# Optimization experiments

Hardware: AMD Instinct MI355X
Metric: run time of the kernel (lower is better)

Reference implementation:

```python
import jax, jax.numpy as jnp
import numpy as np

B, K, N, F, H = 20000, 10, 100000, 256, 128


def setup_inputs() -> dict:
    key = jax.random.key(0)
    ks = jax.random.split(key, 8)
    neighbors = jax.random.randint(ks[0], (B, K), 0, N)
    embed_table = jax.random.normal(ks[1], (N, F), dtype=jnp.float32)
    w = lambda k, shp: jax.random.normal(k, shp, dtype=jnp.float32) * 0.05
    return {
        "neighbors": neighbors,
        "embed_table": embed_table,
        "W1a": w(ks[2], (F, H)), "W1b": w(ks[3], (H, H)),
        "W2a": w(ks[4], (F, H)), "W2b": w(ks[5], (H, H)),
        "W3a": w(ks[6], (F, H)), "W3b": w(ks[7], (H, H)),
    }


def reference(neighbors, embed_table, W1a, W1b, W2a, W2b, W3a, W3b):
    # Gather each batch node's K sampled neighbor embeddings: [B, K, F]
    x = embed_table[neighbors]
    # Three MLP projections: Linear(F,H,no bias) -> tanh -> Linear(H,H,no bias)
    q = jnp.tanh(x @ W1a) @ W1b              # [B, K, H]  (att1)
    k = jnp.tanh(x @ W2a) @ W2b              # [B, K, H]  (att2)
    v = jnp.tanh(x @ W3a) @ W3b              # [B, K, H]  (att3)
    # Per-node attention over the K neighbors, softmax along last dim
    att = jax.nn.softmax(jnp.einsum('bid,bjd->bij', q, k), axis=-1)  # [B, K, K]
    # torch: sum over rows of (att @ v) -> contract both i and j
    out = jnp.einsum('bij,bjd->bd', att, v)  # [B, H]
    return out
```

## Files before the change

### kernel.cpp

```cpp
#include <hip/hip_runtime.h>
#include <hip/hip_bf16.h>

constexpr int B_ = 20000;
constexpr int K_ = 10;
constexpr int N_ = 100000;
constexpr int F_ = 256;
constexpr int H_ = 128;
constexpr int RW = 3 * H_;

typedef __attribute__((ext_vector_type(8))) short bf16x8;
typedef __attribute__((ext_vector_type(4))) float f32x4;
typedef __attribute__((ext_vector_type(4))) unsigned short ushort4v;

__device__ __forceinline__ unsigned short f2bf(float x) {
  unsigned int u = __builtin_bit_cast(unsigned int, x);
  unsigned int r = u + 0x7fffu + ((u >> 16) & 1u);
  return (unsigned short)(r >> 16);
}

__device__ __forceinline__ float bf2f(unsigned int u16) {
  return __builtin_bit_cast(float, u16 << 16);
}

__device__ __forceinline__ float fast_tanh(float x) {
  float e = __expf(2.0f * x);
  return 1.0f - 2.0f * __builtin_amdgcn_rcpf(e + 1.0f);
}

__global__ __launch_bounds__(256) void prep_kernel(
    const float* __restrict__ W1a, const float* __restrict__ W1b,
    const float* __restrict__ W2a, const float* __restrict__ W2b,
    const float* __restrict__ W3a, const float* __restrict__ W3b,
    unsigned short* __restrict__ wat2, unsigned short* __restrict__ wbt2) {
  const float* Wa[3] = {W1a, W2a, W3a};
  const float* Wb[3] = {W1b, W2b, W3b};
  int g = blockIdx.x * 256 + threadIdx.x;
  if (g < 3 * 64 * 512) {
    int chunk = g >> 9;
    int e = g & 511;
    int lane = e >> 3, j = e & 7;
    int c = chunk & 7;
    int ks = (chunk >> 3) & 7;
    int p = chunk >> 6;
    int k = 32 * ks + 8 * (lane >> 4) + j;
    int h = 16 * c + (lane & 15);
    wat2[g] = f2bf(Wa[p][k * H_ + h]);
  } else {
    int g2 = g - 3 * 64 * 512;
    int chunk = g2 >> 9;
    int e = g2 & 511;
    int lane = e >> 3, j = e & 7;
    int ks2 = chunk & 3;
    int c2 = (chunk >> 2) & 7;
    int p = chunk >> 5;
    int k = 32 * ks2 + 8 * (lane >> 4) + j;
    int h2 = 16 * c2 + (lane & 15);
    wbt2[g2] = f2bf(Wb[p][k * H_ + h2]);
  }
}

constexpr int MT = 64;
constexpr int XS = F_ + 8;
constexpr int TS = H_ + 8;

__global__ __launch_bounds__(512, 6) void proj_kernel(
    const float* __restrict__ E,
    const unsigned short* __restrict__ wat2,
    const unsigned short* __restrict__ wbt2,
    unsigned short* __restrict__ qkvI) {
  __shared__ unsigned short xs[MT * XS];
  __shared__ unsigned short ts[MT * TS];

  const int tid = threadIdx.x;
  const int lane = tid & 63;
  const int w = tid >> 6;
  const int l15 = lane & 15;
  const int q = lane >> 4;
  const int row0 = blockIdx.x * MT;

  {
    const float4* Eg = (const float4*)E;
#pragma unroll
    for (int it = 0; it < 8; ++it) {
      int i = tid + 512 * it;
      int r = i >> 6;
      int c4 = i & 63;
      int row = row0 + r;
      if (row >= N_) row = N_ - 1;
      float4 v = Eg[(size_t)row * (F_ / 4) + c4];
      ushort4v o;
      o.x = f2bf(v.x); o.y = f2bf(v.y); o.z = f2bf(v.z); o.w = f2bf(v.w);
      *(ushort4v*)&xs[r * XS + c4 * 4] = o;
    }
  }
  __syncthreads();

  for (int p = 0; p < 3; ++p) {
    const unsigned short* __restrict__ wa = wat2 + p * (64 * 512);
    const unsigned short* __restrict__ wb = wbt2 + p * (32 * 512);

    f32x4 acc[4];
#pragma unroll
    for (int nt = 0; nt < 4; ++nt) acc[nt] = (f32x4)0.0f;

#pragma unroll
    for (int ks = 0; ks < 8; ++ks) {
      bf16x8 af = *(const bf16x8*)&wa[(ks * 8 + w) * 512 + lane * 8];
#pragma unroll
      for (int nt = 0; nt < 4; ++nt) {
        bf16x8 bx = *(const bf16x8*)&xs[(16 * nt + l15) * XS + 32 * ks + 8 * q];
        acc[nt] = __builtin_amdgcn_mfma_f32_16x16x32_bf16(af, bx, acc[nt], 0, 0, 0);
      }
    }

    __syncthreads();
#pragma unroll
    for (int nt = 0; nt < 4; ++nt) {
      ushort4v o;
      o.x = f2bf(fast_tanh(acc[nt][0]));
      o.y = f2bf(fast_tanh(acc[nt][1]));
      o.z = f2bf(fast_tanh(acc[nt][2]));
      o.w = f2bf(fast_tanh(acc[nt][3]));
      *(ushort4v*)&ts[(16 * nt + l15) * TS + 16 * w + 4 * q] = o;
    }
    __syncthreads();

    f32x4 ac2[4];
#pragma unroll
    for (int nt = 0; nt < 4; ++nt) ac2[nt] = (f32x4)0.0f;

#pragma unroll
    for (int ks2 = 0; ks2 < 4; ++ks2) {
      bf16x8 ab = *(const bf16x8*)&wb[(w * 4 + ks2) * 512 + lane * 8];
#pragma unroll
      for (int nt = 0; nt < 4; ++nt) {
        bf16x8 bt = *(const bf16x8*)&ts[(16 * nt + l15) * TS + 32 * ks2 + 8 * q];
        ac2[nt] = __builtin_amdgcn_mfma_f32_16x16x32_bf16(ab, bt, ac2[nt], 0, 0, 0);
      }
    }

#pragma unroll
    for (int nt = 0; nt < 4; ++nt) {
      int n = row0 + 16 * nt + l15;
      if (n < N_) {
        ushort4v o;
        o.x = f2bf(ac2[nt][0]);
        o.y = f2bf(ac2[nt][1]);
        o.z = f2bf(ac2[nt][2]);
        o.w = f2bf(ac2[nt][3]);
        *(ushort4v*)&qkvI[(size_t)n * RW + p * H_ + 16 * w + 4 * q] = o;
      }
    }
  }
}

__global__ __launch_bounds__(256) void agg_kernel(
    const int* __restrict__ nbr,
    const unsigned short* __restrict__ qkvI,
    float* __restrict__ out) {
  const int lane = threadIdx.x & 63;
  const int wv = threadIdx.x >> 6;
  const int b = blockIdx.x * 4 + wv;
  const int l15 = lane & 15;
  const int kg = lane >> 4;

  const int ni = nbr[b * K_ + (l15 < K_ ? l15 : 0)];
  const size_t nbase = (size_t)ni * RW;

  f32x4 sc = (f32x4)0.0f;
#pragma unroll
  for (int k = 0; k < 4; ++k) {
    const int off = k * 32 + kg * 8;
    bf16x8 qf = *(const bf16x8*)&qkvI[nbase + off];
    bf16x8 kf = *(const bf16x8*)&qkvI[nbase + H_ + off];
    sc = __builtin_amdgcn_mfma_f32_16x16x32_bf16(qf, kf, sc, 0, 0, 0);
  }

  if (l15 >= K_) {
#pragma unroll
    for (int r = 0; r < 4; ++r) sc[r] = -3.0e38f;
  }

  float mx[4], e[4], sm[4];
#pragma unroll
  for (int r = 0; r < 4; ++r) mx[r] = sc[r];
#pragma unroll
  for (int st = 1; st < 16; st <<= 1)
#pragma unroll
    for (int r = 0; r < 4; ++r) mx[r] = fmaxf(mx[r], __shfl_xor(mx[r], st, 16));
#pragma unroll
  for (int r = 0; r < 4; ++r) { e[r] = __expf(sc[r] - mx[r]); sm[r] = e[r]; }
#pragma unroll
  for (int st = 1; st < 16; st <<= 1)
#pragma unroll
    for (int r = 0; r < 4; ++r) sm[r] += __shfl_xor(sm[r], st, 16);

  float cs = 0.0f;
#pragma unroll
  for (int r = 0; r < 4; ++r) {
    float a = e[r] * __builtin_amdgcn_rcpf(sm[r]);
    if (kg * 4 + r >= K_) a = 0.0f;
    cs += a;
  }
  cs += __shfl_xor(cs, 16, 64);
  cs += __shfl_xor(cs, 32, 64);

  float o0 = 0.0f, o1 = 0.0f;
#pragma unroll
  for (int j = 0; j < K_; ++j) {
    const float cj = __shfl(cs, j, 64);
    const int nj = __shfl(ni, j, 64);
    const unsigned int v2 =
        *(const unsigned int*)&qkvI[(size_t)nj * RW + 2 * H_ + 2 * lane];
    o0 = fmaf(cj, bf2f(v2 & 0xffffu), o0);
    o1 = fmaf(cj, bf2f(v2 >> 16), o1);
  }
  *(float2*)&out[(size_t)b * H_ + 2 * lane] = make_float2(o0, o1);
}

extern "C" void kernel_launch(void* const* d_in, const int* in_sizes, int n_in,
                              void* d_out, int out_size, void* d_ws, size_t ws_size,
                              hipStream_t stream) {
  const int* nbr = (const int*)d_in[0];
  const float* E = (const float*)d_in[1];
  const float* W1a = (const float*)d_in[2];
  const float* W1b = (const float*)d_in[3];
  const float* W2a = (const float*)d_in[4];
  const float* W2b = (const float*)d_in[5];
  const float* W3a = (const float*)d_in[6];
  const float* W3b = (const float*)d_in[7];
  float* out = (float*)d_out;

  unsigned short* qkvI = (unsigned short*)d_ws;
  unsigned short* wat2 = qkvI + (size_t)N_ * RW;
  unsigned short* wbt2 = wat2 + (size_t)3 * 64 * 512;

  prep_kernel<<<(3 * 64 * 512 + 3 * 32 * 512) / 256, 256, 0, stream>>>(
      W1a, W1b, W2a, W2b, W3a, W3b, wat2, wbt2);
  proj_kernel<<<(N_ + MT - 1) / MT, 512, 0, stream>>>(E, wat2, wbt2, qkvI);
  agg_kernel<<<B_ / 4, 256, 0, stream>>>(nbr, qkvI, out);
}
```

Measured before the change: 236.0 us.

## Software-pipeline projection loop and use packed bf16 conversion instruction

The first-layer GEMM for projection p+1 now runs right after the second-layer GEMM for projection p, so the MFMA work of the next stage overlaps the global stores of the current one and one barrier per iteration is dropped. The manual round-to-nearest bf16 conversion is replaced with the hardware v_cvt_pk_bf16_f32 instruction, which packs two values at once. The launch-bounds occupancy hint of 6 is removed, letting the compiler use more registers at the cost of possibly fewer resident waves.

```diff
diff --git a/kernel.cpp b/kernel.cpp
--- a/kernel.cpp
+++ b/kernel.cpp
@@ -10,7 +10,6 @@
 
 typedef __attribute__((ext_vector_type(8))) short bf16x8;
 typedef __attribute__((ext_vector_type(4))) float f32x4;
-typedef __attribute__((ext_vector_type(4))) unsigned short ushort4v;
 
 __device__ __forceinline__ unsigned short f2bf(float x) {
   unsigned int u = __builtin_bit_cast(unsigned int, x);
@@ -20,6 +19,12 @@
 
 __device__ __forceinline__ float bf2f(unsigned int u16) {
   return __builtin_bit_cast(float, u16 << 16);
+}
+
+__device__ __forceinline__ unsigned int cvt_pk_bf16(float lo, float hi) {
+  unsigned int r;
+  asm("v_cvt_pk_bf16_f32 %0, %1, %2" : "=v"(r) : "v"(lo), "v"(hi));
+  return r;
 }
 
 __device__ __forceinline__ float fast_tanh(float x) {
@@ -63,7 +68,7 @@
 constexpr int XS = F_ + 8;
 constexpr int TS = H_ + 8;
 
-__global__ __launch_bounds__(512, 6) void proj_kernel(
+__global__ __launch_bounds__(512) void proj_kernel(
     const float* __restrict__ E,
     const unsigned short* __restrict__ wat2,
     const unsigned short* __restrict__ wbt2,
@@ -88,21 +93,19 @@
       int row = row0 + r;
       if (row >= N_) row = N_ - 1;
       float4 v = Eg[(size_t)row * (F_ / 4) + c4];
-      ushort4v o;
-      o.x = f2bf(v.x); o.y = f2bf(v.y); o.z = f2bf(v.z); o.w = f2bf(v.w);
-      *(ushort4v*)&xs[r * XS + c4 * 4] = o;
+      unsigned int lo = cvt_pk_bf16(v.x, v.y);
+      unsigned int hi = cvt_pk_bf16(v.z, v.w);
+      *(uint2*)&xs[r * XS + c4 * 4] = make_uint2(lo, hi);
     }
   }
   __syncthreads();
 
-  for (int p = 0; p < 3; ++p) {
-    const unsigned short* __restrict__ wa = wat2 + p * (64 * 512);
-    const unsigned short* __restrict__ wb = wbt2 + p * (32 * 512);
-
-    f32x4 acc[4];
+  f32x4 acc[4];
+
+  {
+    const unsigned short* __restrict__ wa = wat2;
 #pragma unroll
     for (int nt = 0; nt < 4; ++nt) acc[nt] = (f32x4)0.0f;
-
 #pragma unroll
     for (int ks = 0; ks < 8; ++ks) {
       bf16x8 af = *(const bf16x8*)&wa[(ks * 8 + w) * 512 + lane * 8];
@@ -112,23 +115,22 @@
         acc[nt] = __builtin_amdgcn_mfma_f32_16x16x32_bf16(af, bx, acc[nt], 0, 0, 0);
       }
     }
-
-    __syncthreads();
-#pragma unroll
-    for (int nt = 0; nt < 4; ++nt) {
-      ushort4v o;
-      o.x = f2bf(fast_tanh(acc[nt][0]));
-      o.y = f2bf(fast_tanh(acc[nt][1]));
-      o.z = f2bf(fast_tanh(acc[nt][2]));
-      o.w = f2bf(fast_tanh(acc[nt][3]));
-      *(ushort4v*)&ts[(16 * nt + l15) * TS + 16 * w + 4 * q] = o;
-    }
-    __syncthreads();
+  }
+
+#pragma unroll
+  for (int nt = 0; nt < 4; ++nt) {
+    unsigned int lo = cvt_pk_bf16(fast_tanh(acc[nt][0]), fast_tanh(acc[nt][1]));
+    unsigned int hi = cvt_pk_bf16(fast_tanh(acc[nt][2]), fast_tanh(acc[nt][3]));
+    *(uint2*)&ts[(16 * nt + l15) * TS + 16 * w + 4 * q] = make_uint2(lo, hi);
+  }
+  __syncthreads();
+
+  for (int p = 0; p < 3; ++p) {
+    const unsigned short* __restrict__ wb = wbt2 + p * (32 * 512);
 
     f32x4 ac2[4];
 #pragma unroll
     for (int nt = 0; nt < 4; ++nt) ac2[nt] = (f32x4)0.0f;
-
 #pragma unroll
     for (int ks2 = 0; ks2 < 4; ++ks2) {
       bf16x8 ab = *(const bf16x8*)&wb[(w * 4 + ks2) * 512 + lane * 8];
@@ -143,13 +145,36 @@
     for (int nt = 0; nt < 4; ++nt) {
       int n = row0 + 16 * nt + l15;
       if (n < N_) {
-        ushort4v o;
-        o.x = f2bf(ac2[nt][0]);
-        o.y = f2bf(ac2[nt][1]);
-        o.z = f2bf(ac2[nt][2]);
-        o.w = f2bf(ac2[nt][3]);
-        *(ushort4v*)&qkvI[(size_t)n * RW + p * H_ + 16 * w + 4 * q] = o;
-      }
+        unsigned int lo = cvt_pk_bf16(ac2[nt][0], ac2[nt][1]);
+        unsigned int hi = cvt_pk_bf16(ac2[nt][2], ac2[nt][3]);
+        *(uint2*)&qkvI[(size_t)n * RW + p * H_ + 16 * w + 4 * q] =
+            make_uint2(lo, hi);
+      }
+    }
+
+    if (p < 2) {
+      const unsigned short* __restrict__ wa = wat2 + (p + 1) * (64 * 512);
+#pragma unroll
+      for (int nt = 0; nt < 4; ++nt) acc[nt] = (f32x4)0.0f;
+#pragma unroll
+      for (int ks = 0; ks < 8; ++ks) {
+        bf16x8 af = *(const bf16x8*)&wa[(ks * 8 + w) * 512 + lane * 8];
+#pragma unroll
+        for (int nt = 0; nt < 4; ++nt) {
+          bf16x8 bx = *(const bf16x8*)&xs[(16 * nt + l15) * XS + 32 * ks + 8 * q];
+          acc[nt] = __builtin_amdgcn_mfma_f32_16x16x32_bf16(af, bx, acc[nt], 0, 0, 0);
+        }
+      }
+
+      __syncthreads();
+
+#pragma unroll
+      for (int nt = 0; nt < 4; ++nt) {
+        unsigned int lo = cvt_pk_bf16(fast_tanh(acc[nt][0]), fast_tanh(acc[nt][1]));
+        unsigned int hi = cvt_pk_bf16(fast_tanh(acc[nt][2]), fast_tanh(acc[nt][3]));
+        *(uint2*)&ts[(16 * nt + l15) * TS + 16 * w + 4 * q] = make_uint2(lo, hi);
+      }
+      __syncthreads();
     }
   }
 }
```

New measurement: 232.6 us. Within noise of the previous version (-1.5%).
